# Optimization experiments

Hardware: AMD Instinct MI355X
Metric: run time of the kernel (lower is better)

The kernel has to match this reference:

```python
import jax, jax.numpy as jnp
import numpy as np

DIM = 128
HEADS = 8
HD = DIM // HEADS          # 16
KS = 8                     # neighborhood kernel size
STRIDE = 2                 # GNA query-group stride
DIL = 2                    # dilation


def axis_indices(L, k, s, d):
    """Per-axis neighborhood indices [L, k] for dilated, strided, edge-clamped NA.

    Queries are grouped in blocks of `s`; every query in a block shares the
    window of the block's center query (GNA 'stride'). Dilation partitions the
    axis into `d` sub-grids; the window lives on the center query's sub-grid
    and is clamped so it never leaves the axis (natten-style sliding window).
    """
    idx = np.zeros((L, k), dtype=np.int32)
    for i in range(L):
        ic = min((i // s) * s + (s - 1) // 2, L - 1)   # group-center query
        r = ic % d                                      # sub-grid (residue)
        Lsub = (L - r + d - 1) // d                     # sub-grid length
        ii = ic // d                                    # index within sub-grid
        start = min(max(ii - (k - 1) // 2, 0), max(Lsub - k, 0))
        for j in range(k):
            idx[i, j] = r + d * min(start + j, Lsub - 1)
    return idx


def setup_inputs() -> dict:
    key = jax.random.key(0)
    ks = jax.random.split(key, 5)
    x = jax.random.normal(ks[0], (1, DIM, 96, 96), jnp.float32)
    # depthwise-grouped qkv conv: Conv2d(dim, 3*dim, 3, 1, 1, groups=dim)
    qkv_w = jax.random.normal(ks[1], (3 * DIM, 1, 3, 3), jnp.float32) * 0.1
    qkv_b = jax.random.normal(ks[2], (3 * DIM,), jnp.float32) * 0.02
    # 1x1 projection: Conv2d(dim, dim, 1)
    proj_w = jax.random.normal(ks[3], (DIM, DIM, 1, 1), jnp.float32) * (DIM ** -0.5)
    proj_b = jax.random.normal(ks[4], (DIM,), jnp.float32) * 0.02
    return {"x": x, "qkv_w": qkv_w, "qkv_b": qkv_b, "proj_w": proj_w, "proj_b": proj_b}


def reference(x, qkv_w, qkv_b, proj_w, proj_b):
    B, C, H, W = x.shape
    # grouped (groups=C) 3x3 conv producing q,k,v
    qkv = jax.lax.conv_general_dilated(
        x, qkv_w, window_strides=(1, 1), padding=[(1, 1), (1, 1)],
        dimension_numbers=("NCHW", "OIHW", "NCHW"), feature_group_count=C)
    qkv = qkv + qkv_b[None, :, None, None]
    qkv = qkv.reshape(B, 3, C, H, W)

    def to_heads(t):  # b c h w -> b h w nh hd
        return t.reshape(B, HEADS, HD, H, W).transpose(0, 3, 4, 1, 2)

    q = to_heads(qkv[:, 0])
    k = to_heads(qkv[:, 1])
    v = to_heads(qkv[:, 2])

    scale = HD ** -0.5
    ri = jnp.asarray(axis_indices(H, KS, STRIDE, DIL))  # [H, KS]
    ci = jnp.asarray(axis_indices(W, KS, STRIDE, DIL))  # [W, KS]
    R = ri[:, :, None, None]       # [H, KS, 1, 1]
    Cc = ci[None, None, :, :]      # [1, 1, W, KS]
    k_win = k[:, R, Cc]            # [B, H, KS, W, KS, nh, hd]
    v_win = v[:, R, Cc]

    logits = jnp.einsum("bijnd,bipjqnd->bijnpq", q * scale, k_win)
    attn = jax.nn.softmax(logits.reshape(B, H, W, HEADS, KS * KS), axis=-1)
    attn = attn.reshape(B, H, W, HEADS, KS, KS)
    out = jnp.einsum("bijnpq,bipjqnd->bijnd", attn, v_win)

    out = out.transpose(0, 3, 4, 1, 2).reshape(B, C, H, W)  # b h w nh hd -> b c h w
    out = jnp.einsum("bchw,oc->bohw", out, proj_w[:, :, 0, 0]) + proj_b[None, :, None, None]
    return out
```

## Files before the change

kernel.cpp:

```cpp
#include <hip/hip_runtime.h>
#include <hip/hip_bf16.h>

#define HH   96
#define WW   96
#define NPIX 9216
#define CH   128
#define NH   8
#define HD   16
#define KS   8

#define NEPIX   2304
#define QTP  136
#define KVTP 264
#define XP2  61
#define PP3  136

typedef __attribute__((ext_vector_type(8))) short bf16x8;
typedef __attribute__((ext_vector_type(4))) float f32x4;

__device__ __forceinline__ unsigned short f2bf(float f) {
    __hip_bfloat16 b = __float2bfloat16(f);
    union { __hip_bfloat16 b; unsigned short u; } cv; cv.b = b; return cv.u;
}
__device__ __forceinline__ bf16x8 u4_as_bf(uint4 u) {
    union { uint4 u; bf16x8 b; } cv; cv.u = u; return cv.b;
}

__global__ __launch_bounds__(256) void conv_kernel(
    const float* __restrict__ x,
    const float* __restrict__ w,
    const float* __restrict__ bias,
    unsigned short* __restrict__ q_pm,
    unsigned short* __restrict__ k_pm,
    unsigned short* __restrict__ vt_f)
{
    __shared__ float ldsx[128 * XP2];
    __shared__ float wl[3456];
    __shared__ float bl[384];
    __shared__ unsigned short qt [12 * QTP];
    __shared__ unsigned short kvt[ 6 * KVTP];

    const int row = blockIdx.x >> 3;
    const int q8  = blockIdx.x & 7;
    const int j0q = q8 * 12;
    const int tid = threadIdx.x;
    const int g   = tid >> 1;
    const int sh  = tid & 1;
    const bool kvrow = (row & 1) == 0;

    #pragma unroll
    for (int it = 0; it < 12; ++it) {
        const int t = it * 256 + tid;
        if (t < 1920) {
            const int r   = t / 640;
            const int rem = t - r * 640;
            const int c   = rem / 5;
            const int s4  = rem - c * 5;
            const int rg  = row + r - 1;
            const int jj  = j0q - 4 + s4 * 4;
            float4 v = make_float4(0.f, 0.f, 0.f, 0.f);
            if (rg >= 0 && rg < HH && jj >= 0 && jj < WW)
                v = *(const float4*)(x + (size_t)c * NPIX + rg * WW + jj);
            *(float4*)&ldsx[c * XP2 + r * 20 + s4 * 4] = v;
        } else if (t < 2784) {
            const int f = t - 1920;
            *(float4*)&wl[f * 4] = *(const float4*)(w + f * 4);
        } else if (t < 2880) {
            const int f = t - 2784;
            *(float4*)&bl[f * 4] = *(const float4*)(bias + f * 4);
        }
    }
    __syncthreads();

    float xr[3][8];
    {
        const float* xg_l = &ldsx[g * XP2 + 3 + sh * 6];
        #pragma unroll
        for (int dr = 0; dr < 3; ++dr)
            #pragma unroll
            for (int m = 0; m < 8; ++m)
                xr[dr][m] = xg_l[dr * 20 + m];
    }

    #pragma unroll
    for (int dt = 0; dt < 3; ++dt) {
        const int o = 3 * g + dt;
        const int t = o >> 7;
        const int c = o & 127;
        float w9[9];
        #pragma unroll
        for (int k = 0; k < 9; ++k) w9[k] = wl[o * 9 + k];
        const float b = bl[o];

        if (t == 0) {
            #pragma unroll
            for (int px = 0; px < 6; ++px) {
                float acc = b;
                #pragma unroll
                for (int kh = 0; kh < 3; ++kh)
                    #pragma unroll
                    for (int kw = 0; kw < 3; ++kw)
                        acc += xr[kh][px + kw] * w9[kh * 3 + kw];
                qt[(sh * 6 + px) * QTP + c] = f2bf(acc);
            }
        } else if (kvrow) {
            #pragma unroll
            for (int pe = 0; pe < 3; ++pe) {
                const int px = pe * 2;
                float acc = b;
                #pragma unroll
                for (int kh = 0; kh < 3; ++kh)
                    #pragma unroll
                    for (int kw = 0; kw < 3; ++kw)
                        acc += xr[kh][px + kw] * w9[kh * 3 + kw];
                kvt[(sh * 3 + pe) * KVTP + (t - 1) * CH + c] = f2bf(acc);
            }
        }
    }

    __syncthreads();

    const int er = row >> 1;
    const int b6 = j0q >> 1;
    const int ntask = kvrow ? ((q8 == 0) ? 800 : 672) : 192;
    #pragma unroll
    for (int it = 0; it < 4; ++it) {
        const int idx = it * 256 + tid;
        if (idx < 192) {
            const int px = idx >> 4;
            const int c8 = (idx & 15) * 8;
            const int hh = c8 >> 4;
            const int d8 = c8 & 15;
            const uint4 v = *(const uint4*)&qt[px * QTP + c8];
            *(uint4*)(q_pm + ((size_t)hh * NPIX + row * WW + j0q + px) * 16
                      + d8) = v;
        } else if (idx < 288 && kvrow) {
            const int k2  = idx - 192;
            const int epx = k2 >> 4;
            const int c8  = (k2 & 15) * 8;
            const int hh  = c8 >> 4;
            const int d8  = c8 & 15;
            const uint4 v = *(const uint4*)&kvt[epx * KVTP + c8];
            *(uint4*)(k_pm + ((size_t)hh * NEPIX + er * 48 + b6 + epx) * 16
                      + d8) = v;
        } else if (idx < 672 && kvrow) {
            const int v2 = idx - 288;
            const int pr = v2 >> 7;
            const int c  = v2 & 127;
            const int colA  = b6 + pr * 2;
            const int chunk = colA >> 3;
            const int off   = colA & 7;
            const unsigned int a0 =
                (unsigned int)kvt[(pr * 2)     * KVTP + CH + c]
                | ((unsigned int)kvt[(pr * 2 + 1) * KVTP + CH + c] << 16);
            *(unsigned int*)(vt_f
                + (((size_t)(c >> 4) * 48 + er) * 7 + chunk) * 128
                + (c & 15) * 8 + off) = a0;
        } else if (idx < ntask) {
            const int zf = idx - 672;
            const int hh = zf >> 4;
            const int d  = zf & 15;
            *(uint4*)(vt_f + (((size_t)hh * 48 + er) * 7 + 6) * 128 + d * 8)
                = make_uint4(0u, 0u, 0u, 0u);
        }
    }
}

__global__ __launch_bounds__(512, 4) void attn_kernel(
    const unsigned short* __restrict__ q_pm,
    const unsigned short* __restrict__ k_pm,
    const unsigned short* __restrict__ vt_f,
    float* __restrict__ a_t)
{
    __shared__ unsigned short plds[NH][16 * PP3];

    const int seg = blockIdx.x;
    const int i   = seg / 6;
    const int j0  = (seg - i * 6) * 16;
    const int er0 = min(max(i / 2 - 3, 0), 40);
    const int ec0 = min(max(j0 / 2 - 3, 0), 40);
    const int ecs = ec0 >> 3;
    const int sh5 = ec0 & 7;

    const int tid  = threadIdx.x;
    const int h    = tid >> 6;
    const int lane = tid & 63;
    const int nn   = lane & 15;
    const int g    = lane >> 4;
    const int g4   = g * 4;

    const int j   = j0 + nn;
    const int ci0 = min(max(j / 2 - 3, 0), 40) - ec0;

    bf16x8 qf = (bf16x8)(short)0;
    if (g < 2)
        qf = u4_as_bf(*(const uint4*)(q_pm
                + ((size_t)h * NPIX + seg * 16 + nn) * 16 + g * 8));
    const f32x4 zacc = {0.f, 0.f, 0.f, 0.f};
    f32x4 st[8];
    #pragma unroll
    for (int t = 0; t < 8; ++t) {
        bf16x8 kf = (bf16x8)(short)0;
        if (g < 2) {
            const int ep = (er0 + t) * 48 + min(ec0 + nn, 47);
            kf = u4_as_bf(*(const uint4*)(k_pm
                    + ((size_t)h * NEPIX + ep) * 16 + g * 8));
        }
        st[t] = __builtin_amdgcn_mfma_f32_16x16x32_bf16(kf, qf, zacc, 0, 0, 0);
    }

    float m = -1e30f;
    #pragma unroll
    for (int t = 0; t < 8; ++t)
        #pragma unroll
        for (int r = 0; r < 4; ++r) {
            const int cc = g4 + r;
            float T = st[t][r] * 0.25f;
            T = ((unsigned)(cc - ci0) < 8u) ? T : -1e30f;
            st[t][r] = T;
            m = fmaxf(m, T);
        }
    m = fmaxf(m, __shfl_xor(m, 16));
    m = fmaxf(m, __shfl_xor(m, 32));

    float s = 0.f;
    #pragma unroll
    for (int t = 0; t < 8; ++t)
        #pragma unroll
        for (int r = 0; r < 4; ++r) {
            const float p = __expf(st[t][r] - m);
            st[t][r] = p;
            s += p;
        }
    s += __shfl_xor(s, 16);
    s += __shfl_xor(s, 32);

    unsigned short* pr = &plds[h][nn * PP3];
    f32x4 acc = {0.f, 0.f, 0.f, 0.f};

    #pragma unroll
    for (int hf = 0; hf < 2; ++hf) {
        #pragma unroll
        for (int tl = 0; tl < 4; ++tl) {
            const f32x4 P = st[hf * 4 + tl];
            unsigned short hi[4], lo[4];
            #pragma unroll
            for (int r = 0; r < 4; ++r) {
                hi[r] = f2bf(P[r]);
                lo[r] = f2bf(P[r] - __uint_as_float((unsigned)hi[r] << 16));
            }
            *(uint2*)&pr[tl * 16 + g4] =
                make_uint2((unsigned)hi[0] | ((unsigned)hi[1] << 16),
                           (unsigned)hi[2] | ((unsigned)hi[3] << 16));
            *(uint2*)&pr[68 + tl * 16 + g4] =
                make_uint2((unsigned)lo[0] | ((unsigned)lo[1] << 16),
                           (unsigned)lo[2] | ((unsigned)lo[3] << 16));
        }
        #pragma unroll
        for (int ks = 0; ks < 2; ++ks) {
            const int tl = ks * 2 + (g >> 1);
            const int er = er0 + hf * 4 + tl;
            const int ch = ecs + (g & 1);
            const unsigned short* vb = vt_f
                + ((size_t)(h * 48 + er) * 7 + ch) * 128 + nn * 8;
            const uint4 u0 = *(const uint4*)vb;
            bf16x8 vf;
            if (sh5 == 0) {
                vf = u4_as_bf(u0);
            } else {
                const uint4 u1 = *(const uint4*)(vb + 128);
                uint4 o;
                o.x = (u0.z >> 16) | (u0.w << 16);
                o.y = (u0.w >> 16) | (u1.x << 16);
                o.z = (u1.x >> 16) | (u1.y << 16);
                o.w = (u1.y >> 16) | (u1.z << 16);
                vf = u4_as_bf(o);
            }
            const bf16x8 ph =
                u4_as_bf(*(const uint4*)&pr[tl * 16 + (g & 1) * 8]);
            const bf16x8 po =
                u4_as_bf(*(const uint4*)&pr[68 + tl * 16 + (g & 1) * 8]);
            acc = __builtin_amdgcn_mfma_f32_16x16x32_bf16(vf, ph, acc, 0, 0, 0);
            acc = __builtin_amdgcn_mfma_f32_16x16x32_bf16(vf, po, acc, 0, 0, 0);
        }
    }

    const float inv = 1.f / s;
    const int pix = seg * 16 + nn;
    #pragma unroll
    for (int r = 0; r < 4; ++r)
        a_t[(size_t)(h * HD + g4 + r) * NPIX + pix] = acc[r] * inv;
}

__global__ __launch_bounds__(256) void proj_kernel(
    const float* __restrict__ a_t,
    const float* __restrict__ pw,
    const float* __restrict__ pb,
    float* __restrict__ out)
{
    __shared__ float at[CH][36];

    const int tid = threadIdx.x;
    const int px0 = blockIdx.x * 32;

    #pragma unroll
    for (int it = 0; it < 4; ++it) {
        const int idx = it * 256 + tid;
        const int c   = idx >> 3;
        const int p4  = (idx & 7) * 4;
        *(float4*)&at[c][p4] =
            *(const float4*)(a_t + (size_t)c * NPIX + px0 + p4);
    }
    __syncthreads();

    const int og = tid >> 3;
    const int o0 = og * 4;
    const int p0 = (tid & 7) * 4;

    float acc[4][4];
    #pragma unroll
    for (int i = 0; i < 4; ++i) {
        const float b = pb[o0 + i];
        #pragma unroll
        for (int jj = 0; jj < 4; ++jj) acc[i][jj] = b;
    }

    #pragma unroll 2
    for (int c0 = 0; c0 < CH; c0 += 4) {
        float4 wv[4];
        #pragma unroll
        for (int i = 0; i < 4; ++i)
            wv[i] = *(const float4*)(pw + (size_t)(o0 + i) * CH + c0);
        float4 av[4];
        #pragma unroll
        for (int k = 0; k < 4; ++k)
            av[k] = *(const float4*)&at[c0 + k][p0];
        #pragma unroll
        for (int i = 0; i < 4; ++i) {
            acc[i][0] += wv[i].x * av[0].x; acc[i][1] += wv[i].x * av[0].y;
            acc[i][2] += wv[i].x * av[0].z; acc[i][3] += wv[i].x * av[0].w;
            acc[i][0] += wv[i].y * av[1].x; acc[i][1] += wv[i].y * av[1].y;
            acc[i][2] += wv[i].y * av[1].z; acc[i][3] += wv[i].y * av[1].w;
            acc[i][0] += wv[i].z * av[2].x; acc[i][1] += wv[i].z * av[2].y;
            acc[i][2] += wv[i].z * av[2].z; acc[i][3] += wv[i].z * av[2].w;
            acc[i][0] += wv[i].w * av[3].x; acc[i][1] += wv[i].w * av[3].y;
            acc[i][2] += wv[i].w * av[3].z; acc[i][3] += wv[i].w * av[3].w;
        }
    }

    #pragma unroll
    for (int i = 0; i < 4; ++i)
        *(float4*)(out + (size_t)(o0 + i) * NPIX + px0 + p0)
            = make_float4(acc[i][0], acc[i][1], acc[i][2], acc[i][3]);
}

extern "C" void kernel_launch(void* const* d_in, const int* in_sizes, int n_in,
                              void* d_out, int out_size, void* d_ws, size_t ws_size,
                              hipStream_t stream)
{
    const float* x      = (const float*)d_in[0];
    const float* qkv_w  = (const float*)d_in[1];
    const float* qkv_b  = (const float*)d_in[2];
    const float* proj_w = (const float*)d_in[3];
    const float* proj_b = (const float*)d_in[4];
    float* out = (float*)d_out;

    unsigned short* q_pm = (unsigned short*)d_ws;
    unsigned short* k_pm = q_pm + (size_t)NH * NPIX * 16;
    unsigned short* vt_f = k_pm + (size_t)NH * NEPIX * 16;
    float*          a_t  = (float*)(vt_f + (size_t)8 * 48 * 7 * 128);

    conv_kernel<<<768, 256, 0, stream>>>(x, qkv_w, qkv_b, q_pm, k_pm, vt_f);
    attn_kernel<<<576, 512, 0, stream>>>(q_pm, k_pm, vt_f, a_t);
    proj_kernel<<<288, 256, 0, stream>>>(a_t, proj_w, proj_b, out);
}
```

Baseline: 92.98 us.

## Fuse 1x1 projection into attention kernel via shared-memory staging

The attention output tile (128 channels x 16 pixels) now goes to shared memory instead of a global intermediate buffer, and the same block then computes the 1x1 projection and writes the final output. This removes the separate projection launch and the global write and read of the fp32 attention tensor. In exchange the attention kernel uses about 10KB more LDS, which may lower occupancy under launch_bounds(512,4), and each block re-reads the full 64KB weight matrix from global memory or cache.

```diff
diff --git a/kernel.cpp b/kernel.cpp
--- a/kernel.cpp
+++ b/kernel.cpp
@@ -14,6 +14,7 @@
 #define KVTP 264
 #define XP2  61
 #define PP3  136
+#define AOP  20
 
 typedef __attribute__((ext_vector_type(8))) short bf16x8;
 typedef __attribute__((ext_vector_type(4))) float f32x4;
@@ -166,13 +167,16 @@
     }
 }
 
-__global__ __launch_bounds__(512, 4) void attn_kernel(
+__global__ __launch_bounds__(512, 4) void attnproj_kernel(
     const unsigned short* __restrict__ q_pm,
     const unsigned short* __restrict__ k_pm,
     const unsigned short* __restrict__ vt_f,
-    float* __restrict__ a_t)
+    const float* __restrict__ pw,
+    const float* __restrict__ pb,
+    float* __restrict__ out)
 {
     __shared__ unsigned short plds[NH][16 * PP3];
+    __shared__ float ao[CH][AOP];
 
     const int seg = blockIdx.x;
     const int i   = seg / 6;
@@ -286,72 +290,32 @@
     }
 
     const float inv = 1.f / s;
-    const int pix = seg * 16 + nn;
     #pragma unroll
     for (int r = 0; r < 4; ++r)
-        a_t[(size_t)(h * HD + g4 + r) * NPIX + pix] = acc[r] * inv;
-}
-
-__global__ __launch_bounds__(256) void proj_kernel(
-    const float* __restrict__ a_t,
-    const float* __restrict__ pw,
-    const float* __restrict__ pb,
-    float* __restrict__ out)
-{
-    __shared__ float at[CH][36];
-
-    const int tid = threadIdx.x;
-    const int px0 = blockIdx.x * 32;
-
-    #pragma unroll
-    for (int it = 0; it < 4; ++it) {
-        const int idx = it * 256 + tid;
-        const int c   = idx >> 3;
-        const int p4  = (idx & 7) * 4;
-        *(float4*)&at[c][p4] =
-            *(const float4*)(a_t + (size_t)c * NPIX + px0 + p4);
-    }
+        ao[h * HD + g4 + r][nn] = acc[r] * inv;
+
     __syncthreads();
 
-    const int og = tid >> 3;
-    const int o0 = og * 4;
-    const int p0 = (tid & 7) * 4;
-
-    float acc[4][4];
-    #pragma unroll
-    for (int i = 0; i < 4; ++i) {
-        const float b = pb[o0 + i];
-        #pragma unroll
-        for (int jj = 0; jj < 4; ++jj) acc[i][jj] = b;
-    }
-
-    #pragma unroll 2
+    const int o  = tid >> 2;
+    const int p0 = (tid & 3) * 4;
+    const float b = pb[o];
+    float ac[4] = {b, b, b, b};
+
+    #pragma unroll 4
     for (int c0 = 0; c0 < CH; c0 += 4) {
-        float4 wv[4];
-        #pragma unroll
-        for (int i = 0; i < 4; ++i)
-            wv[i] = *(const float4*)(pw + (size_t)(o0 + i) * CH + c0);
-        float4 av[4];
-        #pragma unroll
-        for (int k = 0; k < 4; ++k)
-            av[k] = *(const float4*)&at[c0 + k][p0];
-        #pragma unroll
-        for (int i = 0; i < 4; ++i) {
-            acc[i][0] += wv[i].x * av[0].x; acc[i][1] += wv[i].x * av[0].y;
-            acc[i][2] += wv[i].x * av[0].z; acc[i][3] += wv[i].x * av[0].w;
-            acc[i][0] += wv[i].y * av[1].x; acc[i][1] += wv[i].y * av[1].y;
-            acc[i][2] += wv[i].y * av[1].z; acc[i][3] += wv[i].y * av[1].w;
-            acc[i][0] += wv[i].z * av[2].x; acc[i][1] += wv[i].z * av[2].y;
-            acc[i][2] += wv[i].z * av[2].z; acc[i][3] += wv[i].z * av[2].w;
-            acc[i][0] += wv[i].w * av[3].x; acc[i][1] += wv[i].w * av[3].y;
-            acc[i][2] += wv[i].w * av[3].z; acc[i][3] += wv[i].w * av[3].w;
-        }
-    }
-
-    #pragma unroll
-    for (int i = 0; i < 4; ++i)
-        *(float4*)(out + (size_t)(o0 + i) * NPIX + px0 + p0)
-            = make_float4(acc[i][0], acc[i][1], acc[i][2], acc[i][3]);
+        const float4 wv = *(const float4*)(pw + (size_t)o * CH + c0);
+        const float4 a0 = *(const float4*)&ao[c0 + 0][p0];
+        const float4 a1 = *(const float4*)&ao[c0 + 1][p0];
+        const float4 a2 = *(const float4*)&ao[c0 + 2][p0];
+        const float4 a3 = *(const float4*)&ao[c0 + 3][p0];
+        ac[0] += wv.x * a0.x + wv.y * a1.x + wv.z * a2.x + wv.w * a3.x;
+        ac[1] += wv.x * a0.y + wv.y * a1.y + wv.z * a2.y + wv.w * a3.y;
+        ac[2] += wv.x * a0.z + wv.y * a1.z + wv.z * a2.z + wv.w * a3.z;
+        ac[3] += wv.x * a0.w + wv.y * a1.w + wv.z * a2.w + wv.w * a3.w;
+    }
+
+    *(float4*)(out + (size_t)o * NPIX + seg * 16 + p0)
+        = make_float4(ac[0], ac[1], ac[2], ac[3]);
 }
 
 extern "C" void kernel_launch(void* const* d_in, const int* in_sizes, int n_in,
@@ -368,9 +332,8 @@
     unsigned short* q_pm = (unsigned short*)d_ws;
     unsigned short* k_pm = q_pm + (size_t)NH * NPIX * 16;
     unsigned short* vt_f = k_pm + (size_t)NH * NEPIX * 16;
-    float*          a_t  = (float*)(vt_f + (size_t)8 * 48 * 7 * 128);
 
     conv_kernel<<<768, 256, 0, stream>>>(x, qkv_w, qkv_b, q_pm, k_pm, vt_f);
-    attn_kernel<<<576, 512, 0, stream>>>(q_pm, k_pm, vt_f, a_t);
-    proj_kernel<<<288, 256, 0, stream>>>(a_t, proj_w, proj_b, out);
-}
+    attnproj_kernel<<<576, 512, 0, stream>>>(q_pm, k_pm, vt_f,
+                                             proj_w, proj_b, out);
+}
```

Result: faster. 88.10 us (median of 2 runs) (-5.2%).
